# Optimization experiments

Measured on AMD Instinct MI355X. Metric: run time of the kernel, lower is better.

Reference implementation:

```python
import jax, jax.numpy as jnp
import numpy as np

STRIDE = 1
PADDING = 1
THRESHOLD = 0.5
NAN_FRAC = 0.05


def _conv(x, k, stride):
    return jax.lax.conv_general_dilated(
        x, k, (stride, stride), 'VALID',
        dimension_numbers=('NCHW', 'OIHW', 'NCHW'))


def setup_inputs() -> dict:
    key = jax.random.key(0)
    k1, k2, k3, k4 = jax.random.split(key, 4)
    B, C, H, W = 16, 128, 128, 128
    OC, KH, KW = 256, 3, 3
    x = jax.random.normal(k1, (B, C, H, W), jnp.float32)
    nan_mask = jax.random.uniform(k2, (B, C, H, W)) < NAN_FRAC
    x = jnp.where(nan_mask, jnp.nan, x)
    kernel = jax.random.normal(k3, (OC, C, KH, KW), jnp.float32) * 0.05
    bias = jax.random.normal(k4, (OC,), jnp.float32) * 0.05
    return {"x": x, "kernel": kernel, "bias": bias}


def reference(x, kernel, bias):
    # NaN-aware conv: per-patch nan stats shared across out_channels.
    p = PADDING
    x = jnp.pad(x, ((0, 0), (0, 0), (p, p), (p, p)))  # zero pad (zeros are valid values)
    mask = jnp.isnan(x)
    x0 = jnp.where(mask, jnp.zeros((), x.dtype), x)
    OC, C, KH, KW = kernel.shape
    total = float(C * KH * KW)
    ones = jnp.ones((1, C, KH, KW), x.dtype)
    maskf = mask.astype(x.dtype)
    nan_count = _conv(maskf, ones, STRIDE)      # [B,1,oh,ow]
    val_sum = _conv(x0, ones, STRIDE)           # sum of non-nan values per patch
    valid = total - nan_count
    patch_mean = val_sum / jnp.maximum(valid, 1.0)
    s1 = _conv(x0, kernel, STRIDE)              # conv with NaNs zeroed
    m = _conv(maskf, kernel, STRIDE)            # sum of kernel weights at NaN positions
    out = s1 + patch_mean * m + bias[None, :, None, None]
    bad = nan_count / total >= THRESHOLD        # includes all-NaN patches
    return jnp.where(bad, jnp.nan, out)
```

## Files before the change

### kernel.cpp

```cpp
#include <hip/hip_runtime.h>


typedef __attribute__((ext_vector_type(8))) short bf16x8;
typedef __attribute__((ext_vector_type(4))) float f32x4;

#define HH 128
#define WW 128
#define CC 128

__device__ __forceinline__ unsigned short f2bf(float f) {
    union { float f; unsigned int i; } v; v.f = f;
    unsigned int u = v.i;
    if ((u & 0x7FFFFFFFu) > 0x7F800000u) return (unsigned short)((u >> 16) | 0x0040u);
    unsigned int r = u + 0x7FFFu + ((u >> 16) & 1u);
    return (unsigned short)(r >> 16);
}
__device__ __forceinline__ unsigned int sel2(unsigned int v, unsigned int pmu) {
    unsigned int lo = v & 0xFFFFu, hi = v >> 16;
    if ((lo & 0x7FFFu) > 0x7F80u) lo = pmu;
    if ((hi & 0x7FFFu) > 0x7F80u) hi = pmu;
    return lo | (hi << 16);
}
__device__ __forceinline__ void gl16(const void* g, void* l) {
    __builtin_amdgcn_global_load_lds(
        (const __attribute__((address_space(1))) unsigned int*)g,
        (__attribute__((address_space(3))) unsigned int*)l, 16, 0, 0);
}
#define SBAR() __builtin_amdgcn_sched_barrier(0)

__global__ void k_transpose_stats(const float* __restrict__ x,
                                  unsigned short* __restrict__ xT,
                                  float* __restrict__ cnt,
                                  float* __restrict__ sum, int b0) {
    __shared__ __align__(16) unsigned short ls[128][136];
    int bh = blockIdx.x;
    int bl = bh >> 7, h = bh & 127;
    int b = b0 + bl;
    int w = threadIdx.x;
    const float* xp = x + ((long)b * CC * HH * WW) + h * WW + w;
    int cntv = 0; float sumv = 0.f;
    for (int c8 = 0; c8 < 16; ++c8) {
        unsigned short s8[8];
        #pragma unroll
        for (int j = 0; j < 8; ++j) {
            float fv = xp[(long)(c8 * 8 + j) * (HH * WW)];
            unsigned int bits = __float_as_uint(fv);
            if ((bits & 0x7FFFFFFFu) > 0x7F800000u) { cntv++; s8[j] = 0x7FC0u; }
            else { sumv += fv; s8[j] = f2bf(fv); }
        }
        uint4 p;
        p.x = (unsigned)s8[0] | ((unsigned)s8[1] << 16);
        p.y = (unsigned)s8[2] | ((unsigned)s8[3] << 16);
        p.z = (unsigned)s8[4] | ((unsigned)s8[5] << 16);
        p.w = (unsigned)s8[6] | ((unsigned)s8[7] << 16);
        *(uint4*)&ls[w][c8 * 8] = p;
    }
    cnt[(bh << 7) + w] = (float)cntv;
    sum[(bh << 7) + w] = sumv;
    __syncthreads();
    unsigned short* xb = xT + ((long)bh << 14);
    int ch = w & 15, pw = w >> 4;
    #pragma unroll
    for (int r = 0; r < 16; ++r) {
        int p = (r << 3) + pw;
        *(uint4*)(xb + (p << 7) + (ch << 3)) = *(const uint4*)&ls[p][ch << 3];
    }
}

__global__ void k_patchmean(const float* __restrict__ cnt, const float* __restrict__ sum,
                            unsigned short* __restrict__ pm) {
    int idx = blockIdx.x * 256 + threadIdx.x;
    int ow = idx & 127, oh = (idx >> 7) & 127, bl = idx >> 14;
    float nc = 0.f, vs = 0.f;
    #pragma unroll
    for (int kh = 0; kh < 3; ++kh) {
        int ih = oh + kh - 1; if (ih < 0 || ih >= HH) continue;
        #pragma unroll
        for (int kw = 0; kw < 3; ++kw) {
            int iw = ow + kw - 1; if (iw < 0 || iw >= WW) continue;
            int p = (((bl << 7) + ih) << 7) + iw;
            nc += cnt[p]; vs += sum[p];
        }
    }
    float pmv = vs / fmaxf(1152.f - nc, 1.f);
    unsigned short r = f2bf(pmv);
    if (nc >= 576.f) r = 0x7FC0u;
    pm[idx] = r;
}

__global__ void k_w2(const float* __restrict__ krn, unsigned short* __restrict__ W2) {
    int e = blockIdx.x * 256 + threadIdx.x;
    int s = e & 63;
    int r = (e >> 6) & 255;
    int half = (e >> 14) & 1;
    int khw = e >> 15;
    int c = (half << 6) | (s ^ ((r & 7) << 3));
    W2[e] = f2bf(krn[(r * 128 + c) * 9 + khw]);
}

__global__ __launch_bounds__(512, 2) void k_gemm(
    const unsigned short* __restrict__ xT, const unsigned short* __restrict__ pm,
    const unsigned short* __restrict__ W2, const float* __restrict__ bias,
    float* __restrict__ out, int b0) {
    __shared__ __align__(16) unsigned short lA[2][128 * 64];
    __shared__ __align__(16) unsigned short lB[2][256 * 64];

    int bid = blockIdx.x;
    int oh = bid & 127, bl = bid >> 7;
    int b = b0 + bl;

    int tid = threadIdx.x;
    int lane = tid & 63, wave = tid >> 6;
    int wm = wave >> 2, wn = wave & 3;
    int l15 = lane & 15, quad = lane >> 4;

    int arow = tid >> 2, apart = tid & 3;
    unsigned int pmr = pm[(((bl << 7) + oh) << 7) + arow];

    const char* w2base = (const char*)W2;
    int bsrcoff = (wave << 10) + (lane << 4);
    int bdstoff = (wave << 10);

    f32x4 acc[4][4];
    #pragma unroll
    for (int i = 0; i < 4; ++i)
        #pragma unroll
        for (int j = 0; j < 4; ++j) acc[i][j] = (f32x4)0.f;

    auto issueB = [&](int s, unsigned short* lbbuf) {
        const char* src = w2base + ((long)s << 15) + bsrcoff;
        char* dst = (char*)lbbuf + bdstoff;
        #pragma unroll
        for (int i = 0; i < 4; ++i)
            gl16(src + (i << 13), dst + (i << 13));
    };
    auto loadA = [&](int s, uint4& v0, uint4& v1, unsigned& msk) {
        int khw = s >> 1, c0s = (s & 1) << 6;
        int kh = khw / 3, kw = khw - kh * 3;
        int ih = oh + kh - 1, iw = arow + kw - 1;
        bool valid = ((unsigned)ih < 128u) && ((unsigned)iw < 128u);
        int ihc = ih < 0 ? 0 : (ih > 127 ? 127 : ih);
        int iwc = iw < 0 ? 0 : (iw > 127 ? 127 : iw);
        const uint4* ap = (const uint4*)(xT +
            ((((long)((bl << 7) + ihc) << 7) + iwc) << 7) + c0s + (apart << 4));
        v0 = ap[0];
        v1 = ap[1];
        msk = valid ? 0xFFFFFFFFu : 0u;
    };
    auto stageA = [&](uint4 v0, uint4 v1, unsigned msk, unsigned short* la) {
        v0.x &= msk; v0.y &= msk; v0.z &= msk; v0.w &= msk;
        v1.x &= msk; v1.y &= msk; v1.z &= msk; v1.w &= msk;
        uint4 r0, r1;
        r0.x = sel2(v0.x, pmr); r0.y = sel2(v0.y, pmr);
        r0.z = sel2(v0.z, pmr); r0.w = sel2(v0.w, pmr);
        r1.x = sel2(v1.x, pmr); r1.y = sel2(v1.y, pmr);
        r1.z = sel2(v1.z, pmr); r1.w = sel2(v1.w, pmr);
        char* lar = (char*)la + (arow << 7);
        int sw = (arow & 7) << 4;
        *(uint4*)(lar + (((apart << 5) | 0)  ^ sw)) = r0;
        *(uint4*)(lar + (((apart << 5) | 16) ^ sw)) = r1;
    };
    auto COMPUTE = [&](const unsigned short* la, const unsigned short* lb) {
        int swr = (l15 & 7) << 4;
        #pragma unroll
        for (int ks = 0; ks < 2; ++ks) {
            bf16x8 af[4], bfr[4];
            int cb = ((ks << 6) | (quad << 4)) ^ swr;
            #pragma unroll
            for (int mi = 0; mi < 4; ++mi) {
                int r = (wm << 6) + (mi << 4) + l15;
                af[mi] = *(const bf16x8*)((const char*)la + (r << 7) + cb);
            }
            #pragma unroll
            for (int ni = 0; ni < 4; ++ni) {
                int r = (wn << 6) + (ni << 4) + l15;
                bfr[ni] = *(const bf16x8*)((const char*)lb + (r << 7) + cb);
            }
            #pragma unroll
            for (int mi = 0; mi < 4; ++mi)
                #pragma unroll
                for (int ni = 0; ni < 4; ++ni)
                    acc[mi][ni] = __builtin_amdgcn_mfma_f32_16x16x32_bf16(
                        af[mi], bfr[ni], acc[mi][ni], 0, 0, 0);
        }
    };

    uint4 av0[2], av1[2]; unsigned am[2];

    issueB(0, lB[0]); SBAR();
    loadA(0, av0[0], av1[0], am[0]); SBAR();
    loadA(1, av0[1], av1[1], am[1]); SBAR();
    asm volatile("s_waitcnt vmcnt(2)" ::: "memory");
    SBAR();
    stageA(av0[0], av1[0], am[0], lA[0]);
    asm volatile("s_waitcnt lgkmcnt(0)" ::: "memory");
    SBAR();
    __builtin_amdgcn_s_barrier();
    SBAR();

    #pragma unroll
    for (int s = 0; s < 18; ++s) {
        const int cur = s & 1, nxt = cur ^ 1;
        if (s < 17) { issueB(s + 1, lB[nxt]); SBAR(); }
        if (s < 16) { loadA(s + 2, av0[cur], av1[cur], am[cur]); SBAR(); }
        if (s < 16)      { asm volatile("s_waitcnt vmcnt(6)" ::: "memory"); }
        else if (s == 16){ asm volatile("s_waitcnt vmcnt(4)" ::: "memory"); }
        SBAR();
        if (s < 17) stageA(av0[nxt], av1[nxt], am[nxt], lA[nxt]);
        COMPUTE(lA[cur], lB[cur]);
        if (s < 17) {
            if (s < 16) { asm volatile("s_waitcnt vmcnt(2) lgkmcnt(0)" ::: "memory"); }
            else        { asm volatile("s_waitcnt vmcnt(0) lgkmcnt(0)" ::: "memory"); }
            SBAR();
            __builtin_amdgcn_s_barrier();
            SBAR();
        }
    }

    #pragma unroll
    for (int ni = 0; ni < 4; ++ni) {
        int oc = (wn << 6) + (ni << 4) + l15;
        float bv = bias[oc];
        float* op = out + ((long)((b << 8) + oc) * 128 + oh) * 128;
        #pragma unroll
        for (int mi = 0; mi < 4; ++mi) {
            int ow0 = (wm << 6) + (mi << 4) + (quad << 2);
            float4 o;
            o.x = acc[mi][ni][0] + bv;
            o.y = acc[mi][ni][1] + bv;
            o.z = acc[mi][ni][2] + bv;
            o.w = acc[mi][ni][3] + bv;
            *(float4*)(op + ow0) = o;
        }
    }
}

extern "C" void kernel_launch(void* const* d_in, const int* in_sizes, int n_in,
                              void* d_out, int out_size, void* d_ws, size_t ws_size,
                              hipStream_t stream) {
    const float* x    = (const float*)d_in[0];
    const float* krn  = (const float*)d_in[1];
    const float* bias = (const float*)d_in[2];
    float* out = (float*)d_out;

    const size_t W2_BYTES = 294912ull * 2;
    int G = 16;
    while (G > 1) {
        size_t need = W2_BYTES + 256
                    + (size_t)G * (16384ull * 128 * 2)
                    + (size_t)G * (16384ull * 4) * 2
                    + (size_t)G * (16384ull * 2)
                    + 1024;
        if (need <= ws_size) break;
        G >>= 1;
    }

    char* ws = (char*)d_ws;
    size_t off = 0;
    auto carve = [&](size_t bytes) { char* p = ws + off; off += (bytes + 255) & ~255ull; return p; };
    unsigned short* W2  = (unsigned short*)carve(W2_BYTES);
    unsigned short* xT  = (unsigned short*)carve((size_t)G * 16384 * 128 * 2);
    float*          cnt = (float*)carve((size_t)G * 16384 * 4);
    float*          sum = (float*)carve((size_t)G * 16384 * 4);
    unsigned short* pm  = (unsigned short*)carve((size_t)G * 16384 * 2);

    k_w2<<<dim3(1152), dim3(256), 0, stream>>>(krn, W2);
    for (int b0 = 0; b0 < 16; b0 += G) {
        k_transpose_stats<<<dim3(G * 128), dim3(128), 0, stream>>>(x, xT, cnt, sum, b0);
        k_patchmean<<<dim3(G * 64), dim3(256), 0, stream>>>(cnt, sum, pm);
        k_gemm<<<dim3(G * 128), dim3(512), 0, stream>>>(xT, pm, W2, bias, out, b0);
    }
}
```

Measured before the change: 657.4 us.

## Shrink GEMM tile to 64x256 with K-step 32 and four blocks per CU

Restructures the implicit-GEMM conv kernel: each block now covers half an output row (64 pixels) and all 256 output channels using 256 threads, with K chunks of 32 channels instead of 64. The LDS layout, swizzle, pre-packed weight layout and pipeline wait counts change to match, and there are twice as many blocks and stages. The aim is higher occupancy and smaller LDS use per block. The cost is that weight tiles are reloaded twice as often per output row, and each stage does less work per barrier.

```diff
diff --git a/kernel.cpp b/kernel.cpp
--- a/kernel.cpp
+++ b/kernel.cpp
@@ -90,36 +90,39 @@
 
 __global__ void k_w2(const float* __restrict__ krn, unsigned short* __restrict__ W2) {
     int e = blockIdx.x * 256 + threadIdx.x;
-    int s = e & 63;
-    int r = (e >> 6) & 255;
-    int half = (e >> 14) & 1;
+    int j = e & 7;
+    int c2 = (e >> 3) & 3;
+    int r = (e >> 5) & 255;
+    int kq = (e >> 13) & 3;
     int khw = e >> 15;
-    int c = (half << 6) | (s ^ ((r & 7) << 3));
+    int c = (kq << 5) + ((c2 ^ ((r >> 1) & 3)) << 3) + j;
     W2[e] = f2bf(krn[(r * 128 + c) * 9 + khw]);
 }
 
-__global__ __launch_bounds__(512, 2) void k_gemm(
+__global__ __launch_bounds__(256, 4) void k_gemm(
     const unsigned short* __restrict__ xT, const unsigned short* __restrict__ pm,
     const unsigned short* __restrict__ W2, const float* __restrict__ bias,
     float* __restrict__ out, int b0) {
-    __shared__ __align__(16) unsigned short lA[2][128 * 64];
-    __shared__ __align__(16) unsigned short lB[2][256 * 64];
+    __shared__ __align__(16) unsigned short lA[2][64 * 32];
+    __shared__ __align__(16) unsigned short lB[2][256 * 32];
 
     int bid = blockIdx.x;
-    int oh = bid & 127, bl = bid >> 7;
-    int b = b0 + bl;
+    int ow0 = (bid & 1) << 6;
+    int oh  = (bid >> 1) & 127;
+    int bl  = bid >> 8;
+    int b   = b0 + bl;
 
     int tid = threadIdx.x;
     int lane = tid & 63, wave = tid >> 6;
-    int wm = wave >> 2, wn = wave & 3;
     int l15 = lane & 15, quad = lane >> 4;
 
     int arow = tid >> 2, apart = tid & 3;
-    unsigned int pmr = pm[(((bl << 7) + oh) << 7) + arow];
+    int ow = ow0 + arow;
+    unsigned int pmr = pm[(((bl << 7) + oh) << 7) + ow];
 
     const char* w2base = (const char*)W2;
-    int bsrcoff = (wave << 10) + (lane << 4);
-    int bdstoff = (wave << 10);
+    int bsrcoff = (wave << 12) + (lane << 4);
+    int bdstoff = (wave << 12);
 
     f32x4 acc[4][4];
     #pragma unroll
@@ -128,88 +131,74 @@
         for (int j = 0; j < 4; ++j) acc[i][j] = (f32x4)0.f;
 
     auto issueB = [&](int s, unsigned short* lbbuf) {
-        const char* src = w2base + ((long)s << 15) + bsrcoff;
+        const char* src = w2base + ((long)s << 14) + bsrcoff;
         char* dst = (char*)lbbuf + bdstoff;
         #pragma unroll
         for (int i = 0; i < 4; ++i)
-            gl16(src + (i << 13), dst + (i << 13));
-    };
-    auto loadA = [&](int s, uint4& v0, uint4& v1, unsigned& msk) {
-        int khw = s >> 1, c0s = (s & 1) << 6;
+            gl16(src + (i << 10), dst + (i << 10));
+    };
+    auto loadA = [&](int s, uint4& v, unsigned& msk) {
+        int khw = s >> 2, kq = s & 3;
         int kh = khw / 3, kw = khw - kh * 3;
-        int ih = oh + kh - 1, iw = arow + kw - 1;
+        int ih = oh + kh - 1, iw = ow + kw - 1;
         bool valid = ((unsigned)ih < 128u) && ((unsigned)iw < 128u);
         int ihc = ih < 0 ? 0 : (ih > 127 ? 127 : ih);
         int iwc = iw < 0 ? 0 : (iw > 127 ? 127 : iw);
-        const uint4* ap = (const uint4*)(xT +
-            ((((long)((bl << 7) + ihc) << 7) + iwc) << 7) + c0s + (apart << 4));
-        v0 = ap[0];
-        v1 = ap[1];
+        v = *(const uint4*)(xT + ((((long)((bl << 7) + ihc) << 7) + iwc) << 7)
+                            + (kq << 5) + (apart << 3));
         msk = valid ? 0xFFFFFFFFu : 0u;
     };
-    auto stageA = [&](uint4 v0, uint4 v1, unsigned msk, unsigned short* la) {
-        v0.x &= msk; v0.y &= msk; v0.z &= msk; v0.w &= msk;
-        v1.x &= msk; v1.y &= msk; v1.z &= msk; v1.w &= msk;
-        uint4 r0, r1;
-        r0.x = sel2(v0.x, pmr); r0.y = sel2(v0.y, pmr);
-        r0.z = sel2(v0.z, pmr); r0.w = sel2(v0.w, pmr);
-        r1.x = sel2(v1.x, pmr); r1.y = sel2(v1.y, pmr);
-        r1.z = sel2(v1.z, pmr); r1.w = sel2(v1.w, pmr);
-        char* lar = (char*)la + (arow << 7);
-        int sw = (arow & 7) << 4;
-        *(uint4*)(lar + (((apart << 5) | 0)  ^ sw)) = r0;
-        *(uint4*)(lar + (((apart << 5) | 16) ^ sw)) = r1;
+    auto stageA = [&](uint4 v, unsigned msk, unsigned short* la) {
+        v.x &= msk; v.y &= msk; v.z &= msk; v.w &= msk;
+        uint4 r0;
+        r0.x = sel2(v.x, pmr); r0.y = sel2(v.y, pmr);
+        r0.z = sel2(v.z, pmr); r0.w = sel2(v.w, pmr);
+        char* dst = (char*)la + (arow << 6) + ((apart ^ ((arow >> 1) & 3)) << 4);
+        *(uint4*)dst = r0;
     };
     auto COMPUTE = [&](const unsigned short* la, const unsigned short* lb) {
-        int swr = (l15 & 7) << 4;
-        #pragma unroll
-        for (int ks = 0; ks < 2; ++ks) {
-            bf16x8 af[4], bfr[4];
-            int cb = ((ks << 6) | (quad << 4)) ^ swr;
+        int cb = (quad ^ ((l15 >> 1) & 3)) << 4;
+        bf16x8 af[4], bfr[4];
+        #pragma unroll
+        for (int mi = 0; mi < 4; ++mi)
+            af[mi] = *(const bf16x8*)((const char*)la + (((mi << 4) + l15) << 6) + cb);
+        #pragma unroll
+        for (int ni = 0; ni < 4; ++ni)
+            bfr[ni] = *(const bf16x8*)((const char*)lb +
+                       (((wave << 6) + (ni << 4) + l15) << 6) + cb);
+        #pragma unroll
+        for (int mi = 0; mi < 4; ++mi)
             #pragma unroll
-            for (int mi = 0; mi < 4; ++mi) {
-                int r = (wm << 6) + (mi << 4) + l15;
-                af[mi] = *(const bf16x8*)((const char*)la + (r << 7) + cb);
-            }
-            #pragma unroll
-            for (int ni = 0; ni < 4; ++ni) {
-                int r = (wn << 6) + (ni << 4) + l15;
-                bfr[ni] = *(const bf16x8*)((const char*)lb + (r << 7) + cb);
-            }
-            #pragma unroll
-            for (int mi = 0; mi < 4; ++mi)
-                #pragma unroll
-                for (int ni = 0; ni < 4; ++ni)
-                    acc[mi][ni] = __builtin_amdgcn_mfma_f32_16x16x32_bf16(
-                        af[mi], bfr[ni], acc[mi][ni], 0, 0, 0);
-        }
-    };
-
-    uint4 av0[2], av1[2]; unsigned am[2];
+            for (int ni = 0; ni < 4; ++ni)
+                acc[mi][ni] = __builtin_amdgcn_mfma_f32_16x16x32_bf16(
+                    af[mi], bfr[ni], acc[mi][ni], 0, 0, 0);
+    };
+
+    uint4 av[2]; unsigned am[2];
 
     issueB(0, lB[0]); SBAR();
-    loadA(0, av0[0], av1[0], am[0]); SBAR();
-    loadA(1, av0[1], av1[1], am[1]); SBAR();
-    asm volatile("s_waitcnt vmcnt(2)" ::: "memory");
+    loadA(0, av[0], am[0]); SBAR();
+    loadA(1, av[1], am[1]); SBAR();
+    asm volatile("s_waitcnt vmcnt(1)" ::: "memory");
     SBAR();
-    stageA(av0[0], av1[0], am[0], lA[0]);
+    stageA(av[0], am[0], lA[0]);
     asm volatile("s_waitcnt lgkmcnt(0)" ::: "memory");
     SBAR();
     __builtin_amdgcn_s_barrier();
     SBAR();
 
     #pragma unroll
-    for (int s = 0; s < 18; ++s) {
+    for (int s = 0; s < 36; ++s) {
         const int cur = s & 1, nxt = cur ^ 1;
-        if (s < 17) { issueB(s + 1, lB[nxt]); SBAR(); }
-        if (s < 16) { loadA(s + 2, av0[cur], av1[cur], am[cur]); SBAR(); }
-        if (s < 16)      { asm volatile("s_waitcnt vmcnt(6)" ::: "memory"); }
-        else if (s == 16){ asm volatile("s_waitcnt vmcnt(4)" ::: "memory"); }
+        if (s < 35) { issueB(s + 1, lB[nxt]); SBAR(); }
+        if (s < 34) { loadA(s + 2, av[cur], am[cur]); SBAR(); }
+        if (s < 34)      { asm volatile("s_waitcnt vmcnt(5)" ::: "memory"); }
+        else if (s == 34){ asm volatile("s_waitcnt vmcnt(4)" ::: "memory"); }
         SBAR();
-        if (s < 17) stageA(av0[nxt], av1[nxt], am[nxt], lA[nxt]);
+        if (s < 35) stageA(av[nxt], am[nxt], lA[nxt]);
         COMPUTE(lA[cur], lB[cur]);
-        if (s < 17) {
-            if (s < 16) { asm volatile("s_waitcnt vmcnt(2) lgkmcnt(0)" ::: "memory"); }
+        if (s < 35) {
+            if (s < 34) { asm volatile("s_waitcnt vmcnt(1) lgkmcnt(0)" ::: "memory"); }
             else        { asm volatile("s_waitcnt vmcnt(0) lgkmcnt(0)" ::: "memory"); }
             SBAR();
             __builtin_amdgcn_s_barrier();
@@ -219,18 +208,18 @@
 
     #pragma unroll
     for (int ni = 0; ni < 4; ++ni) {
-        int oc = (wn << 6) + (ni << 4) + l15;
+        int oc = (wave << 6) + (ni << 4) + l15;
         float bv = bias[oc];
-        float* op = out + ((long)((b << 8) + oc) * 128 + oh) * 128;
+        float* op = out + ((long)((b << 8) + oc) * 128 + oh) * 128 + ow0;
         #pragma unroll
         for (int mi = 0; mi < 4; ++mi) {
-            int ow0 = (wm << 6) + (mi << 4) + (quad << 2);
+            int og = (mi << 4) + (quad << 2);
             float4 o;
             o.x = acc[mi][ni][0] + bv;
             o.y = acc[mi][ni][1] + bv;
             o.z = acc[mi][ni][2] + bv;
             o.w = acc[mi][ni][3] + bv;
-            *(float4*)(op + ow0) = o;
+            *(float4*)(op + og) = o;
         }
     }
 }
@@ -268,6 +257,6 @@
     for (int b0 = 0; b0 < 16; b0 += G) {
         k_transpose_stats<<<dim3(G * 128), dim3(128), 0, stream>>>(x, xT, cnt, sum, b0);
         k_patchmean<<<dim3(G * 64), dim3(256), 0, stream>>>(cnt, sum, pm);
-        k_gemm<<<dim3(G * 128), dim3(512), 0, stream>>>(xT, pm, W2, bias, out, b0);
-    }
-}
+        k_gemm<<<dim3(G * 256), dim3(256), 0, stream>>>(xT, pm, W2, bias, out, b0);
+    }
+}
```

Result: faster. 619.5 us (-5.8%).
